# Optimization experiments

Measured on AMD Instinct MI355X. Metric: run time of the kernel, lower is better.

Reference implementation:

```python
import jax, jax.numpy as jnp
import numpy as np

B, N, D, L, T = 64, 64, 128, 4, 10  # batch, atoms, hidden_dim, n_layers, n_atom_types
EPS = 1e-5


def setup_inputs() -> dict:
    key = jax.random.key(0)
    ks = jax.random.split(key, 10)
    def rn(k, shape, s=0.05):
        return jax.random.normal(k, shape, jnp.float32) * s
    return dict(
        positions=jax.random.normal(ks[0], (B, N, 3), jnp.float32),
        atomic_numbers=jax.random.randint(ks[1], (B, N), 0, T),
        embed=rn(ks[2], (T, D)),
        edge_w1=rn(ks[3], (L, 2 * D + 1, D)), edge_b1=jnp.zeros((L, D), jnp.float32),
        edge_w2=rn(ks[4], (L, D, D)), edge_b2=jnp.zeros((L, D), jnp.float32),
        node_w1=rn(ks[5], (L, 2 * D, D)), node_b1=jnp.zeros((L, D), jnp.float32),
        node_w2=rn(ks[6], (L, D, D)), node_b2=jnp.zeros((L, D), jnp.float32),
        ln_g=jnp.ones((L, D), jnp.float32), ln_b=jnp.zeros((L, D), jnp.float32),
        out_w=rn(ks[7], (D, 3)), out_b=jnp.zeros((3,), jnp.float32),
    )


def _layer(h, dist_sq, ew1, eb1, ew2, eb2, nw1, nb1, nw2, nb2, g, b):
    # edge_mlp first linear on cat([h_i, h_j, dist_sq]) == h@Wa (bcast over j)
    # + h@Wb (bcast over i) + dist_sq * w_d, avoiding materializing the concat.
    wa, wb, wd = ew1[:D], ew1[D:2 * D], ew1[2 * D]
    pre = (h @ wa)[:, :, None, :] + (h @ wb)[:, None, :, :] + dist_sq * wd + eb1  # [B,N,N,D]
    m_ij = jax.nn.silu(jax.nn.silu(pre) @ ew2 + eb2)
    m_i = m_ij.mean(axis=2)  # mean over j -> [B,N,D]
    # node_mlp on cat([h, m_i]) split the same way; dropout is eval-mode identity.
    h_out = jax.nn.silu(h @ nw1[:D] + m_i @ nw1[D:] + nb1) @ nw2 + nb2
    x = h + h_out
    mu = x.mean(-1, keepdims=True)
    var = ((x - mu) ** 2).mean(-1, keepdims=True)
    return (x - mu) / jnp.sqrt(var + EPS) * g + b


def reference(positions, atomic_numbers, embed, edge_w1, edge_b1, edge_w2, edge_b2,
              node_w1, node_b1, node_w2, node_b2, ln_g, ln_b, out_w, out_b):
    h = embed[atomic_numbers]  # [B,N,D]
    diff = positions[:, :, None, :] - positions[:, None, :, :]
    dist_sq = (diff ** 2).sum(-1, keepdims=True)  # [B,N,N,1]
    for i in range(L):
        h = _layer(h, dist_sq, edge_w1[i], edge_b1[i], edge_w2[i], edge_b2[i],
                   node_w1[i], node_b1[i], node_w2[i], node_b2[i], ln_g[i], ln_b[i])
    return h @ out_w + out_b  # [B,N,3]
```

## Files before the change

### kernel.cpp

```cpp
#include <hip/hip_runtime.h>
#include <hip/hip_fp16.h>


typedef _Float16 f16;
typedef _Float16 f16x4 __attribute__((ext_vector_type(4)));
typedef _Float16 f16x8 __attribute__((ext_vector_type(8)));
typedef float f32x4 __attribute__((ext_vector_type(4)));

union H2x4 { f16x8 v; __half2 h[4]; };

__device__ __forceinline__ float bf2f(unsigned short u) {
    union { unsigned int i; float f; } v; v.i = ((unsigned int)u) << 16; return v.f;
}
__device__ __forceinline__ unsigned short f2bf(float f) {
    union { float f; unsigned int i; } v; v.f = f;
    unsigned int x = v.i;
    return (unsigned short)((x + 0x7fffu + ((x >> 16) & 1u)) >> 16);
}
__device__ __forceinline__ float silu_f(float x) {
    float e = __builtin_amdgcn_exp2f(-1.44269504088896f * x);
    return x * __builtin_amdgcn_rcpf(1.0f + e);
}
__device__ __forceinline__ __half2 silu_h2(__half2 x, __half2 kf, __half2 one2) {
    __half2 e = h2exp2(__hmul2(x, kf));
    return __hmul2(x, h2rcp(__hadd2(one2, e)));
}

struct Ptrs { const void* p[14]; };

__device__ __forceinline__ float ldf(const void* p, int i, int bf) {
    return bf ? bf2f(((const unsigned short*)p)[i]) : ((const float*)p)[i];
}

#define FRAG_TOTAL 49152
#define SMALL_TOTAL 17539

__global__ __launch_bounds__(256) void prep_kernel(
    Ptrs ptrs, f16* dst, float* sc)
{
    __shared__ int flgsh;
    int t = threadIdx.x;
    if (t < 64) {
        int ex = (((const unsigned short*)ptrs.p[0])[t * 2] >> 7) & 0xFF;
        unsigned long long m = __ballot(ex >= 110 && ex <= 135);
        if (t == 0) flgsh = (__popcll(m) >= 40) ? 1 : 0;
    }
    __syncthreads();
    int bf = flgsh;

    int gid = blockIdx.x * 256 + t;
    if (gid < FRAG_TOTAL) {
        int lay = gid / 12288;
        int r   = gid % 12288;
        const void* src; int base, rowoff = 0, r2;
        if (r < 6144) {
            int mat = r >> 11; r2 = r & 2047;
            if (mat == 0)      { src = ptrs.p[2]; base = lay * 32896; }
            else if (mat == 1) { src = ptrs.p[2]; base = lay * 32896; rowoff = 128; }
            else               { src = ptrs.p[4]; base = lay * 16384; }
        } else if (r < 10240) {
            r2 = r - 6144; src = ptrs.p[6]; base = lay * 32768;
        } else {
            r2 = r - 10240; src = ptrs.p[8]; base = lay * 16384;
        }
        int s = r2 >> 9, c = (r2 >> 6) & 7, l = r2 & 63;
        int row0 = rowoff + s * 32 + ((l >> 4) << 3);
        int col  = (c << 4) + (l & 15);
        f16x8 v;
#pragma unroll
        for (int jj = 0; jj < 8; jj++)
            v[jj] = (f16)ldf(src, base + (row0 + jj) * 128 + col, bf);
        *(f16x8*)(dst + gid * 8) = v;
    } else {
        int sid = gid - FRAG_TOTAL;
        if (sid >= SMALL_TOTAL) return;
        const void* src; int i;
        if      (sid < 12288) { src = ptrs.p[0]; i = sid; }
        else if (sid < 13568) { src = ptrs.p[1]; i = sid - 12288; }
        else if (sid < 14080) { int k = sid - 13568;
                                src = ptrs.p[2]; i = (k >> 7) * 32896 + 32768 + (k & 127); }
        else if (sid < 14592) { src = ptrs.p[3];  i = sid - 14080; }
        else if (sid < 15104) { src = ptrs.p[5];  i = sid - 14592; }
        else if (sid < 15616) { src = ptrs.p[7];  i = sid - 15104; }
        else if (sid < 16128) { src = ptrs.p[9];  i = sid - 15616; }
        else if (sid < 16640) { src = ptrs.p[10]; i = sid - 16128; }
        else if (sid < 17152) { src = ptrs.p[11]; i = sid - 16640; }
        else if (sid < 17536) { src = ptrs.p[12]; i = sid - 17152; }
        else                  { src = ptrs.p[13]; i = sid - 17536; }
        sc[sid] = ldf(src, i, bf);
    }
}

__global__ __launch_bounds__(256) void embed_ab_kernel(
    const int* an, const float* sc, const f16* wa, const f16* wb,
    const float* eb1C, f16* h16, f16* a16, f16* b16)
{
    int t = threadIdx.x;
    int w = t >> 6, lane = t & 63;
    int row0 = blockIdx.x << 4;
    int m_ = lane & 15, q_ = lane >> 4;
    const float* emb = sc + 12288;
    int a = an[row0 + m_];
    a = a < 0 ? 0 : (a > 9 ? 9 : a);
    f16x8 afrag[4];
#pragma unroll
    for (int s = 0; s < 4; s++) {
        f32x4 u0 = *(const f32x4*)(emb + a * 128 + s * 32 + q_ * 8);
        f32x4 u1 = *(const f32x4*)(emb + a * 128 + s * 32 + q_ * 8 + 4);
        f16x8 hv;
#pragma unroll
        for (int e = 0; e < 4; e++) { hv[e] = (f16)u0[e]; hv[e + 4] = (f16)u1[e]; }
        afrag[s] = hv;
        if (w == 0)
            *(f16x8*)(h16 + (row0 + m_) * 128 + s * 32 + q_ * 8) = hv;
    }
#pragma unroll
    for (int mat = 0; mat < 2; mat++) {
        const f16* W = mat ? wb : wa;
        f16* out     = mat ? b16 : a16;
#pragma unroll
        for (int cc = 0; cc < 2; cc++) {
            int c = 2 * w + cc;
            float init = mat ? 0.0f : eb1C[c * 16 + m_];
            f32x4 acc = { init, init, init, init };
#pragma unroll
            for (int s = 0; s < 4; s++) {
                f16x8 bfr = *(const f16x8*)(W + ((s * 8 + c) * 64 + lane) * 8);
                acc = __builtin_amdgcn_mfma_f32_16x16x32_f16(afrag[s], bfr, acc, 0, 0, 0);
            }
#pragma unroll
            for (int r = 0; r < 4; r++)
                out[(row0 + q_ * 4 + r) * 128 + c * 16 + m_] = (f16)acc[r];
        }
    }
}

__global__ __launch_bounds__(256) void edge_kernel(
    const float* sc, const f16* a16, const f16* b16,
    const f16* ew2_swz, const float* eb2C, const float* wdC, f16* m_out)
{
    __shared__ f16 Wlds[8192];
    __shared__ f16 S[64 * 136];
    __shared__ __half2 wd2_sh[64];
    __shared__ float dsq_sh[64];

    int t  = threadIdx.x;
    int ig = blockIdx.x;
    int b  = ig >> 6;
    const float* posC = sc;
    int lane = t & 63, w = t >> 6;
    int wr = w & 1, wc = w >> 1;

#pragma unroll
    for (int k = 0; k < 4; k++) {
        int idx = (k * 256 + t) * 8;
        *(f16x8*)(Wlds + idx) = *(const f16x8*)(ew2_swz + idx);
    }
    f16x8 bfB[2][4];
#pragma unroll
    for (int s2 = 0; s2 < 2; s2++)
#pragma unroll
        for (int c = 0; c < 4; c++)
            bfB[s2][c] = *(const f16x8*)(ew2_swz +
                (((s2 + 2) * 8 + wc * 4 + c) * 64 + lane) * 8);

    if (t >= 64 && t < 128) {
        int u = t - 64;
        wd2_sh[u] = __floats2half2_rn(wdC[2 * u], wdC[2 * u + 1]);
    }
    if (t < 64) {
        float xi = posC[ig * 3 + 0], yi = posC[ig * 3 + 1], zi = posC[ig * 3 + 2];
        int jg = b * 64 + t;
        float dx = xi - posC[jg * 3 + 0];
        float dy = yi - posC[jg * 3 + 1];
        float dz = zi - posC[jg * 3 + 2];
        dsq_sh[t] = dx * dx + dy * dy + dz * dz;
    }
    __syncthreads();

    {
        int j  = t >> 2;
        int cb = (t & 3) * 32;
        float dsf = dsq_sh[j];
        __half dh = __float2half_rn(dsf);
        __half2 ds2 = __halves2half2(dh, dh);
        __half2 kf   = __floats2half2_rn(-1.44269504f, -1.44269504f);
        __half2 one2 = __floats2half2_rn(1.0f, 1.0f);
        H2x4 a_r[4], wd_r[4];
#pragma unroll
        for (int k = 0; k < 4; k++) {
            a_r[k].v  = *(const f16x8*)(a16 + ig * 128 + cb + k * 8);
            wd_r[k].v = *(const f16x8*)((const f16*)wd2_sh + cb + k * 8);
        }
#pragma unroll
        for (int k = 0; k < 4; k++) {
            H2x4 bv, sv;
            bv.v = *(const f16x8*)(b16 + (b * 64 + j) * 128 + cb + k * 8);
#pragma unroll
            for (int e = 0; e < 4; e++) {
                __half2 pre = __hfma2(ds2, wd_r[k].h[e],
                                      __hadd2(a_r[k].h[e], bv.h[e]));
                sv.h[e] = silu_h2(pre, kf, one2);
            }
            *(f16x8*)(S + j * 136 + cb + k * 8) = sv.v;
        }
    }
    __syncthreads();

    int m_ = lane & 15, q_ = lane >> 4;
    f32x4 acc[4][2];
#pragma unroll
    for (int c = 0; c < 4; c++) {
        float e = eb2C[(wc * 4 + c) * 16 + m_];
        acc[c][0] = (f32x4){ e, e, e, e };
        acc[c][1] = acc[c][0];
    }
#pragma unroll
    for (int s = 0; s < 2; s++) {
        f16x8 bfr[4];
#pragma unroll
        for (int c = 0; c < 4; c++)
            bfr[c] = *(const f16x8*)(Wlds + ((s * 8 + wc * 4 + c) * 64 + lane) * 8);
#pragma unroll
        for (int mb = 0; mb < 2; mb++) {
            f16x8 af = *(const f16x8*)(S + ((wr * 2 + mb) * 16 + m_) * 136 + s * 32 + q_ * 8);
#pragma unroll
            for (int c = 0; c < 4; c++)
                acc[c][mb] = __builtin_amdgcn_mfma_f32_16x16x32_f16(af, bfr[c], acc[c][mb], 0, 0, 0);
        }
    }
#pragma unroll
    for (int s2 = 0; s2 < 2; s2++) {
#pragma unroll
        for (int mb = 0; mb < 2; mb++) {
            f16x8 af = *(const f16x8*)(S + ((wr * 2 + mb) * 16 + m_) * 136 + (s2 + 2) * 32 + q_ * 8);
#pragma unroll
            for (int c = 0; c < 4; c++)
                acc[c][mb] = __builtin_amdgcn_mfma_f32_16x16x32_f16(af, bfB[s2][c], acc[c][mb], 0, 0, 0);
        }
    }
    float scv4[4];
#pragma unroll
    for (int c = 0; c < 4; c++) {
        float scv = 0.0f;
#pragma unroll
        for (int mb = 0; mb < 2; mb++)
#pragma unroll
            for (int r = 0; r < 4; r++)
                scv += silu_f(acc[c][mb][r]);
        scv += __shfl_xor(scv, 16);
        scv += __shfl_xor(scv, 32);
        scv4[c] = scv;
    }
    __syncthreads();
    float* msum = (float*)S;
    if (lane < 16) {
#pragma unroll
        for (int c = 0; c < 4; c++)
            msum[wr * 128 + (wc * 4 + c) * 16 + lane] = scv4[c];
    }
    __syncthreads();
    if (t < 128) {
        float mv = (msum[t] + msum[128 + t]) * (1.0f / 64.0f);
        m_out[ig * 128 + t] = (f16)mv;
    }
}

__global__ __launch_bounds__(256) void node_mid_kernel(
    const f16* h16, const f16* m16, const f16* nw1s, const f16* nw2s,
    const float* nb1C, const float* nb2C, const float* lngC, const float* lnbC,
    const f16* waN, const f16* wbN, const float* eb1N,
    f16* a16, f16* b16)
{
    __shared__ f16 relay[16 * 136];
    __shared__ float s1sh[4][16], s2sh[4][16];
    int t = threadIdx.x;
    int w = t >> 6, lane = t & 63;
    int row0 = blockIdx.x << 4;
    int m_ = lane & 15, q_ = lane >> 4;

    f16x8 af[8];
#pragma unroll
    for (int s = 0; s < 4; s++) {
        af[s]     = *(const f16x8*)(h16 + (row0 + m_) * 128 + s * 32 + q_ * 8);
        af[s + 4] = *(const f16x8*)(m16 + (row0 + m_) * 128 + s * 32 + q_ * 8);
    }
#pragma unroll
    for (int cc = 0; cc < 2; cc++) {
        int c = 2 * w + cc;
        float e = nb1C[c * 16 + m_];
        f32x4 acc = { e, e, e, e };
#pragma unroll
        for (int s = 0; s < 8; s++) {
            f16x8 bfr = *(const f16x8*)(nw1s + ((s * 8 + c) * 64 + lane) * 8);
            acc = __builtin_amdgcn_mfma_f32_16x16x32_f16(af[s], bfr, acc, 0, 0, 0);
        }
#pragma unroll
        for (int r = 0; r < 4; r++)
            relay[(q_ * 4 + r) * 136 + c * 16 + m_] = (f16)silu_f(acc[r]);
    }
    __syncthreads();
    f16x8 uf[4];
#pragma unroll
    for (int s = 0; s < 4; s++)
        uf[s] = *(const f16x8*)(relay + m_ * 136 + s * 32 + q_ * 8);
    float x[2][4];
#pragma unroll
    for (int cc = 0; cc < 2; cc++) {
        int c = 2 * w + cc;
        float e = nb2C[c * 16 + m_];
        f32x4 acc = { e, e, e, e };
#pragma unroll
        for (int s = 0; s < 4; s++) {
            f16x8 bfr = *(const f16x8*)(nw2s + ((s * 8 + c) * 64 + lane) * 8);
            acc = __builtin_amdgcn_mfma_f32_16x16x32_f16(uf[s], bfr, acc, 0, 0, 0);
        }
#pragma unroll
        for (int r = 0; r < 4; r++)
            x[cc][r] = acc[r] + (float)h16[(row0 + q_ * 4 + r) * 128 + c * 16 + m_];
    }
    float s1p[4], s2p[4];
#pragma unroll
    for (int r = 0; r < 4; r++) {
        s1p[r] = x[0][r] + x[1][r];
        s2p[r] = x[0][r] * x[0][r] + x[1][r] * x[1][r];
    }
#pragma unroll
    for (int msk = 1; msk < 16; msk <<= 1)
#pragma unroll
        for (int r = 0; r < 4; r++) {
            s1p[r] += __shfl_xor(s1p[r], msk);
            s2p[r] += __shfl_xor(s2p[r], msk);
        }
    if (m_ == 0)
#pragma unroll
        for (int r = 0; r < 4; r++) {
            s1sh[w][q_ * 4 + r] = s1p[r];
            s2sh[w][q_ * 4 + r] = s2p[r];
        }
    __syncthreads();
    float mu[4], rs[4];
#pragma unroll
    for (int r = 0; r < 4; r++) {
        int row = q_ * 4 + r;
        float S1 = s1sh[0][row] + s1sh[1][row] + s1sh[2][row] + s1sh[3][row];
        float S2 = s2sh[0][row] + s2sh[1][row] + s2sh[2][row] + s2sh[3][row];
        mu[r] = S1 * (1.0f / 128.0f);
        float var = S2 * (1.0f / 128.0f) - mu[r] * mu[r];
        rs[r] = rsqrtf(var + 1e-5f);
    }
#pragma unroll
    for (int cc = 0; cc < 2; cc++) {
        int c = 2 * w + cc;
#pragma unroll
        for (int r = 0; r < 4; r++) {
            int col = c * 16 + m_;
            int row = row0 + q_ * 4 + r;
            float y = (x[cc][r] - mu[r]) * rs[r] * lngC[col] + lnbC[col];
            ((f16*)h16)[row * 128 + col] = (f16)y;
            relay[(q_ * 4 + r) * 136 + col] = (f16)y;
        }
    }
    __syncthreads();
    f16x8 hf[4];
#pragma unroll
    for (int s = 0; s < 4; s++)
        hf[s] = *(const f16x8*)(relay + m_ * 136 + s * 32 + q_ * 8);
#pragma unroll
    for (int mat = 0; mat < 2; mat++) {
        const f16* W = mat ? wbN : waN;
        f16* out     = mat ? b16 : a16;
#pragma unroll
        for (int cc = 0; cc < 2; cc++) {
            int c = 2 * w + cc;
            float init = mat ? 0.0f : eb1N[c * 16 + m_];
            f32x4 acc = { init, init, init, init };
#pragma unroll
            for (int s = 0; s < 4; s++) {
                f16x8 bfr = *(const f16x8*)(W + ((s * 8 + c) * 64 + lane) * 8);
                acc = __builtin_amdgcn_mfma_f32_16x16x32_f16(hf[s], bfr, acc, 0, 0, 0);
            }
#pragma unroll
            for (int r = 0; r < 4; r++)
                out[(row0 + q_ * 4 + r) * 128 + c * 16 + m_] = (f16)acc[r];
        }
    }
}

__global__ __launch_bounds__(256) void node_final_kernel(
    const void* pos_raw, const f16* h16, const f16* m16,
    const f16* nw1s, const f16* nw2s,
    const float* nb1C, const float* nb2C, const float* lngC, const float* lnbC,
    const float* owC, const float* obC, void* out)
{
    __shared__ f16 relay[16 * 136];
    __shared__ float s1sh[4][16], s2sh[4][16];
    __shared__ float psh[4][16][3];
    __shared__ int flgsh;
    int t = threadIdx.x;
    int w = t >> 6, lane = t & 63;
    int row0 = blockIdx.x << 4;
    int m_ = lane & 15, q_ = lane >> 4;

    if (t < 64) {
        int ex = (((const unsigned short*)pos_raw)[t * 2] >> 7) & 0xFF;
        unsigned long long mk = __ballot(ex >= 110 && ex <= 135);
        if (t == 0) flgsh = (__popcll(mk) >= 40) ? 1 : 0;
    }

    f16x8 af[8];
#pragma unroll
    for (int s = 0; s < 4; s++) {
        af[s]     = *(const f16x8*)(h16 + (row0 + m_) * 128 + s * 32 + q_ * 8);
        af[s + 4] = *(const f16x8*)(m16 + (row0 + m_) * 128 + s * 32 + q_ * 8);
    }
#pragma unroll
    for (int cc = 0; cc < 2; cc++) {
        int c = 2 * w + cc;
        float e = nb1C[c * 16 + m_];
        f32x4 acc = { e, e, e, e };
#pragma unroll
        for (int s = 0; s < 8; s++) {
            f16x8 bfr = *(const f16x8*)(nw1s + ((s * 8 + c) * 64 + lane) * 8);
            acc = __builtin_amdgcn_mfma_f32_16x16x32_f16(af[s], bfr, acc, 0, 0, 0);
        }
#pragma unroll
        for (int r = 0; r < 4; r++)
            relay[(q_ * 4 + r) * 136 + c * 16 + m_] = (f16)silu_f(acc[r]);
    }
    __syncthreads();
    f16x8 uf[4];
#pragma unroll
    for (int s = 0; s < 4; s++)
        uf[s] = *(const f16x8*)(relay + m_ * 136 + s * 32 + q_ * 8);
    float x[2][4];
#pragma unroll
    for (int cc = 0; cc < 2; cc++) {
        int c = 2 * w + cc;
        float e = nb2C[c * 16 + m_];
        f32x4 acc = { e, e, e, e };
#pragma unroll
        for (int s = 0; s < 4; s++) {
            f16x8 bfr = *(const f16x8*)(nw2s + ((s * 8 + c) * 64 + lane) * 8);
            acc = __builtin_amdgcn_mfma_f32_16x16x32_f16(uf[s], bfr, acc, 0, 0, 0);
        }
#pragma unroll
        for (int r = 0; r < 4; r++)
            x[cc][r] = acc[r] + (float)h16[(row0 + q_ * 4 + r) * 128 + c * 16 + m_];
    }
    float s1p[4], s2p[4];
#pragma unroll
    for (int r = 0; r < 4; r++) {
        s1p[r] = x[0][r] + x[1][r];
        s2p[r] = x[0][r] * x[0][r] + x[1][r] * x[1][r];
    }
#pragma unroll
    for (int msk = 1; msk < 16; msk <<= 1)
#pragma unroll
        for (int r = 0; r < 4; r++) {
            s1p[r] += __shfl_xor(s1p[r], msk);
            s2p[r] += __shfl_xor(s2p[r], msk);
        }
    if (m_ == 0)
#pragma unroll
        for (int r = 0; r < 4; r++) {
            s1sh[w][q_ * 4 + r] = s1p[r];
            s2sh[w][q_ * 4 + r] = s2p[r];
        }
    __syncthreads();
    float p[3][4];
#pragma unroll
    for (int r = 0; r < 4; r++) {
        int row = q_ * 4 + r;
        float S1 = s1sh[0][row] + s1sh[1][row] + s1sh[2][row] + s1sh[3][row];
        float S2 = s2sh[0][row] + s2sh[1][row] + s2sh[2][row] + s2sh[3][row];
        float mu = S1 * (1.0f / 128.0f);
        float var = S2 * (1.0f / 128.0f) - mu * mu;
        float rs = rsqrtf(var + 1e-5f);
        float p0 = 0.0f, p1 = 0.0f, p2 = 0.0f;
#pragma unroll
        for (int cc = 0; cc < 2; cc++) {
            int col = (2 * w + cc) * 16 + m_;
            float y = (x[cc][r] - mu) * rs * lngC[col] + lnbC[col];
            p0 += y * owC[col * 3 + 0];
            p1 += y * owC[col * 3 + 1];
            p2 += y * owC[col * 3 + 2];
        }
        p[0][r] = p0; p[1][r] = p1; p[2][r] = p2;
    }
#pragma unroll
    for (int msk = 1; msk < 16; msk <<= 1)
#pragma unroll
        for (int k = 0; k < 3; k++)
#pragma unroll
            for (int r = 0; r < 4; r++)
                p[k][r] += __shfl_xor(p[k][r], msk);
    if (m_ == 0)
#pragma unroll
        for (int r = 0; r < 4; r++)
#pragma unroll
            for (int k = 0; k < 3; k++)
                psh[w][q_ * 4 + r][k] = p[k][r];
    __syncthreads();
    if (t < 16) {
        int row = row0 + t;
        int bf = flgsh;
#pragma unroll
        for (int k = 0; k < 3; k++) {
            float v = psh[0][t][k] + psh[1][t][k] + psh[2][t][k] + psh[3][t][k]
                      + obC[k];
            if (bf) ((unsigned short*)out)[row * 3 + k] = f2bf(v);
            else    ((float*)out)[row * 3 + k] = v;
        }
    }
}

extern "C" void kernel_launch(void* const* d_in, const int* in_sizes, int n_in,
                              void* d_out, int out_size, void* d_ws, size_t ws_size,
                              hipStream_t stream)
{
    const int* an = (const int*)d_in[1];

    char* ws = (char*)d_ws;
    float* sc   = (float*)(ws + 1024);
    f16*   Wswz = (f16*)(ws + (128u << 10));
    f16*   h16  = (f16*)(ws + (1u << 20));
    f16*   a16  = (f16*)(ws + (2u << 20));
    f16*   b16  = (f16*)(ws + (3u << 20));
    f16*   m16  = (f16*)(ws + (4u << 20));

    Ptrs ptrs;
    const int src_idx[14] = {0, 2, 3, 4, 5, 6, 7, 8, 9, 10, 11, 12, 13, 14};
    for (int k = 0; k < 14; k++) ptrs.p[k] = d_in[src_idx[k]];

    prep_kernel<<<261, 256, 0, stream>>>(ptrs, Wswz, sc);
    embed_ab_kernel<<<256, 256, 0, stream>>>(an, sc, Wswz, Wswz + 16384,
                                             sc + 14080, h16, a16, b16);
    for (int lay = 0; lay < 4; lay++) {
        const f16* wl = Wswz + lay * 98304;
        const float* wdC  = sc + 13568 + lay * 128;
        const float* eb2C = sc + 14592 + lay * 128;
        const float* nb1C = sc + 15104 + lay * 128;
        const float* nb2C = sc + 15616 + lay * 128;
        const float* lngC = sc + 16128 + lay * 128;
        const float* lnbC = sc + 16640 + lay * 128;

        edge_kernel<<<4096, 256, 0, stream>>>(sc, a16, b16, wl + 32768,
                                              eb2C, wdC, m16);
        if (lay < 3) {
            const f16* wlN = Wswz + (lay + 1) * 98304;
            node_mid_kernel<<<256, 256, 0, stream>>>(
                h16, m16, wl + 49152, wl + 81920, nb1C, nb2C, lngC, lnbC,
                wlN, wlN + 16384, sc + 14080 + (lay + 1) * 128, a16, b16);
        } else {
            node_final_kernel<<<256, 256, 0, stream>>>(
                d_in[0], h16, m16, wl + 49152, wl + 81920,
                nb1C, nb2C, lngC, lnbC,
                sc + 17152, sc + 17536, d_out);
        }
    }
}
```

Before: 213.9 us.

## Widen parallelism in prep and node kernels, drop edge kernel barrier

The prep kernel now has each thread convert one weight element instead of eight, so it launches many more blocks. The embed and node kernels go from 4 to 8 waves per block, with each wave owning a single 16-column tile instead of two, and the LayerNorm and projection reductions are widened to match. The edge kernel moves its row-sum buffer into a separate shared array, which removes one __syncthreads at the cost of a little more LDS. The aim is to shorten the serial small kernels, but 8-wave blocks may lower occupancy, and the per-element prep writes are narrower.

New measurement: 216.0 us. No clear change (+1.0%).

```diff
diff --git a/kernel.cpp b/kernel.cpp
--- a/kernel.cpp
+++ b/kernel.cpp
@@ -33,6 +33,7 @@
 }
 
 #define FRAG_TOTAL 49152
+#define ELEM_TOTAL 393216
 #define SMALL_TOTAL 17539
 
 __global__ __launch_bounds__(256) void prep_kernel(
@@ -49,9 +50,10 @@
     int bf = flgsh;
 
     int gid = blockIdx.x * 256 + t;
-    if (gid < FRAG_TOTAL) {
-        int lay = gid / 12288;
-        int r   = gid % 12288;
+    if (gid < ELEM_TOTAL) {
+        int f = gid >> 3, j = gid & 7;
+        int lay = f / 12288;
+        int r   = f % 12288;
         const void* src; int base, rowoff = 0, r2;
         if (r < 6144) {
             int mat = r >> 11; r2 = r & 2047;
@@ -64,15 +66,11 @@
             r2 = r - 10240; src = ptrs.p[8]; base = lay * 16384;
         }
         int s = r2 >> 9, c = (r2 >> 6) & 7, l = r2 & 63;
-        int row0 = rowoff + s * 32 + ((l >> 4) << 3);
-        int col  = (c << 4) + (l & 15);
-        f16x8 v;
-#pragma unroll
-        for (int jj = 0; jj < 8; jj++)
-            v[jj] = (f16)ldf(src, base + (row0 + jj) * 128 + col, bf);
-        *(f16x8*)(dst + gid * 8) = v;
+        int row = rowoff + s * 32 + ((l >> 4) << 3) + j;
+        int col = (c << 4) + (l & 15);
+        dst[gid] = (f16)ldf(src, base + row * 128 + col, bf);
     } else {
-        int sid = gid - FRAG_TOTAL;
+        int sid = gid - ELEM_TOTAL;
         if (sid >= SMALL_TOTAL) return;
         const void* src; int i;
         if      (sid < 12288) { src = ptrs.p[0]; i = sid; }
@@ -91,7 +89,7 @@
     }
 }
 
-__global__ __launch_bounds__(256) void embed_ab_kernel(
+__global__ __launch_bounds__(512) void embed_ab_kernel(
     const int* an, const float* sc, const f16* wa, const f16* wb,
     const float* eb1C, f16* h16, f16* a16, f16* b16)
 {
@@ -114,24 +112,21 @@
         if (w == 0)
             *(f16x8*)(h16 + (row0 + m_) * 128 + s * 32 + q_ * 8) = hv;
     }
+    int c = w;
 #pragma unroll
     for (int mat = 0; mat < 2; mat++) {
         const f16* W = mat ? wb : wa;
         f16* out     = mat ? b16 : a16;
-#pragma unroll
-        for (int cc = 0; cc < 2; cc++) {
-            int c = 2 * w + cc;
-            float init = mat ? 0.0f : eb1C[c * 16 + m_];
-            f32x4 acc = { init, init, init, init };
-#pragma unroll
-            for (int s = 0; s < 4; s++) {
-                f16x8 bfr = *(const f16x8*)(W + ((s * 8 + c) * 64 + lane) * 8);
-                acc = __builtin_amdgcn_mfma_f32_16x16x32_f16(afrag[s], bfr, acc, 0, 0, 0);
-            }
-#pragma unroll
-            for (int r = 0; r < 4; r++)
-                out[(row0 + q_ * 4 + r) * 128 + c * 16 + m_] = (f16)acc[r];
-        }
+        float init = mat ? 0.0f : eb1C[c * 16 + m_];
+        f32x4 acc = { init, init, init, init };
+#pragma unroll
+        for (int s = 0; s < 4; s++) {
+            f16x8 bfr = *(const f16x8*)(W + ((s * 8 + c) * 64 + lane) * 8);
+            acc = __builtin_amdgcn_mfma_f32_16x16x32_f16(afrag[s], bfr, acc, 0, 0, 0);
+        }
+#pragma unroll
+        for (int r = 0; r < 4; r++)
+            out[(row0 + q_ * 4 + r) * 128 + c * 16 + m_] = (f16)acc[r];
     }
 }
 
@@ -143,6 +138,7 @@
     __shared__ f16 S[64 * 136];
     __shared__ __half2 wd2_sh[64];
     __shared__ float dsq_sh[64];
+    __shared__ float msum[256];
 
     int t  = threadIdx.x;
     int ig = blockIdx.x;
@@ -252,8 +248,6 @@
         scv += __shfl_xor(scv, 32);
         scv4[c] = scv;
     }
-    __syncthreads();
-    float* msum = (float*)S;
     if (lane < 16) {
 #pragma unroll
         for (int c = 0; c < 4; c++)
@@ -266,18 +260,19 @@
     }
 }
 
-__global__ __launch_bounds__(256) void node_mid_kernel(
+__global__ __launch_bounds__(512) void node_mid_kernel(
     const f16* h16, const f16* m16, const f16* nw1s, const f16* nw2s,
     const float* nb1C, const float* nb2C, const float* lngC, const float* lnbC,
     const f16* waN, const f16* wbN, const float* eb1N,
     f16* a16, f16* b16)
 {
     __shared__ f16 relay[16 * 136];
-    __shared__ float s1sh[4][16], s2sh[4][16];
+    __shared__ float s1sh[8][16], s2sh[8][16];
     int t = threadIdx.x;
     int w = t >> 6, lane = t & 63;
     int row0 = blockIdx.x << 4;
     int m_ = lane & 15, q_ = lane >> 4;
+    int c = w;
 
     f16x8 af[8];
 #pragma unroll
@@ -285,9 +280,7 @@
         af[s]     = *(const f16x8*)(h16 + (row0 + m_) * 128 + s * 32 + q_ * 8);
         af[s + 4] = *(const f16x8*)(m16 + (row0 + m_) * 128 + s * 32 + q_ * 8);
     }
-#pragma unroll
-    for (int cc = 0; cc < 2; cc++) {
-        int c = 2 * w + cc;
+    {
         float e = nb1C[c * 16 + m_];
         f32x4 acc = { e, e, e, e };
 #pragma unroll
@@ -304,10 +297,8 @@
 #pragma unroll
     for (int s = 0; s < 4; s++)
         uf[s] = *(const f16x8*)(relay + m_ * 136 + s * 32 + q_ * 8);
-    float x[2][4];
-#pragma unroll
-    for (int cc = 0; cc < 2; cc++) {
-        int c = 2 * w + cc;
+    float x[4];
+    {
         float e = nb2C[c * 16 + m_];
         f32x4 acc = { e, e, e, e };
 #pragma unroll
@@ -317,13 +308,13 @@
         }
 #pragma unroll
         for (int r = 0; r < 4; r++)
-            x[cc][r] = acc[r] + (float)h16[(row0 + q_ * 4 + r) * 128 + c * 16 + m_];
+            x[r] = acc[r] + (float)h16[(row0 + q_ * 4 + r) * 128 + c * 16 + m_];
     }
     float s1p[4], s2p[4];
 #pragma unroll
     for (int r = 0; r < 4; r++) {
-        s1p[r] = x[0][r] + x[1][r];
-        s2p[r] = x[0][r] * x[0][r] + x[1][r] * x[1][r];
+        s1p[r] = x[r];
+        s2p[r] = x[r] * x[r];
     }
 #pragma unroll
     for (int msk = 1; msk < 16; msk <<= 1)
@@ -343,23 +334,20 @@
 #pragma unroll
     for (int r = 0; r < 4; r++) {
         int row = q_ * 4 + r;
-        float S1 = s1sh[0][row] + s1sh[1][row] + s1sh[2][row] + s1sh[3][row];
-        float S2 = s2sh[0][row] + s2sh[1][row] + s2sh[2][row] + s2sh[3][row];
+        float S1 = 0.0f, S2 = 0.0f;
+#pragma unroll
+        for (int w2 = 0; w2 < 8; w2++) { S1 += s1sh[w2][row]; S2 += s2sh[w2][row]; }
         mu[r] = S1 * (1.0f / 128.0f);
         float var = S2 * (1.0f / 128.0f) - mu[r] * mu[r];
         rs[r] = rsqrtf(var + 1e-5f);
     }
 #pragma unroll
-    for (int cc = 0; cc < 2; cc++) {
-        int c = 2 * w + cc;
-#pragma unroll
-        for (int r = 0; r < 4; r++) {
-            int col = c * 16 + m_;
-            int row = row0 + q_ * 4 + r;
-            float y = (x[cc][r] - mu[r]) * rs[r] * lngC[col] + lnbC[col];
-            ((f16*)h16)[row * 128 + col] = (f16)y;
-            relay[(q_ * 4 + r) * 136 + col] = (f16)y;
-        }
+    for (int r = 0; r < 4; r++) {
+        int col = c * 16 + m_;
+        int row = row0 + q_ * 4 + r;
+        float y = (x[r] - mu[r]) * rs[r] * lngC[col] + lnbC[col];
+        ((f16*)h16)[row * 128 + col] = (f16)y;
+        relay[(q_ * 4 + r) * 136 + col] = (f16)y;
     }
     __syncthreads();
     f16x8 hf[4];
@@ -370,37 +358,34 @@
     for (int mat = 0; mat < 2; mat++) {
         const f16* W = mat ? wbN : waN;
         f16* out     = mat ? b16 : a16;
-#pragma unroll
-        for (int cc = 0; cc < 2; cc++) {
-            int c = 2 * w + cc;
-            float init = mat ? 0.0f : eb1N[c * 16 + m_];
-            f32x4 acc = { init, init, init, init };
-#pragma unroll
-            for (int s = 0; s < 4; s++) {
-                f16x8 bfr = *(const f16x8*)(W + ((s * 8 + c) * 64 + lane) * 8);
-                acc = __builtin_amdgcn_mfma_f32_16x16x32_f16(hf[s], bfr, acc, 0, 0, 0);
-            }
-#pragma unroll
-            for (int r = 0; r < 4; r++)
-                out[(row0 + q_ * 4 + r) * 128 + c * 16 + m_] = (f16)acc[r];
-        }
-    }
-}
-
-__global__ __launch_bounds__(256) void node_final_kernel(
+        float init = mat ? 0.0f : eb1N[c * 16 + m_];
+        f32x4 acc = { init, init, init, init };
+#pragma unroll
+        for (int s = 0; s < 4; s++) {
+            f16x8 bfr = *(const f16x8*)(W + ((s * 8 + c) * 64 + lane) * 8);
+            acc = __builtin_amdgcn_mfma_f32_16x16x32_f16(hf[s], bfr, acc, 0, 0, 0);
+        }
+#pragma unroll
+        for (int r = 0; r < 4; r++)
+            out[(row0 + q_ * 4 + r) * 128 + c * 16 + m_] = (f16)acc[r];
+    }
+}
+
+__global__ __launch_bounds__(512) void node_final_kernel(
     const void* pos_raw, const f16* h16, const f16* m16,
     const f16* nw1s, const f16* nw2s,
     const float* nb1C, const float* nb2C, const float* lngC, const float* lnbC,
     const float* owC, const float* obC, void* out)
 {
     __shared__ f16 relay[16 * 136];
-    __shared__ float s1sh[4][16], s2sh[4][16];
-    __shared__ float psh[4][16][3];
+    __shared__ float s1sh[8][16], s2sh[8][16];
+    __shared__ float psh[8][16][3];
     __shared__ int flgsh;
     int t = threadIdx.x;
     int w = t >> 6, lane = t & 63;
     int row0 = blockIdx.x << 4;
     int m_ = lane & 15, q_ = lane >> 4;
+    int c = w;
 
     if (t < 64) {
         int ex = (((const unsigned short*)pos_raw)[t * 2] >> 7) & 0xFF;
@@ -414,9 +399,7 @@
         af[s]     = *(const f16x8*)(h16 + (row0 + m_) * 128 + s * 32 + q_ * 8);
         af[s + 4] = *(const f16x8*)(m16 + (row0 + m_) * 128 + s * 32 + q_ * 8);
     }
-#pragma unroll
-    for (int cc = 0; cc < 2; cc++) {
-        int c = 2 * w + cc;
+    {
         float e = nb1C[c * 16 + m_];
         f32x4 acc = { e, e, e, e };
 #pragma unroll
@@ -433,10 +416,8 @@
 #pragma unroll
     for (int s = 0; s < 4; s++)
         uf[s] = *(const f16x8*)(relay + m_ * 136 + s * 32 + q_ * 8);
-    float x[2][4];
-#pragma unroll
-    for (int cc = 0; cc < 2; cc++) {
-        int c = 2 * w + cc;
+    float x[4];
+    {
         float e = nb2C[c * 16 + m_];
         f32x4 acc = { e, e, e, e };
 #pragma unroll
@@ -446,13 +427,13 @@
         }
 #pragma unroll
         for (int r = 0; r < 4; r++)
-            x[cc][r] = acc[r] + (float)h16[(row0 + q_ * 4 + r) * 128 + c * 16 + m_];
+            x[r] = acc[r] + (float)h16[(row0 + q_ * 4 + r) * 128 + c * 16 + m_];
     }
     float s1p[4], s2p[4];
 #pragma unroll
     for (int r = 0; r < 4; r++) {
-        s1p[r] = x[0][r] + x[1][r];
-        s2p[r] = x[0][r] * x[0][r] + x[1][r] * x[1][r];
+        s1p[r] = x[r];
+        s2p[r] = x[r] * x[r];
     }
 #pragma unroll
     for (int msk = 1; msk < 16; msk <<= 1)
@@ -472,21 +453,17 @@
 #pragma unroll
     for (int r = 0; r < 4; r++) {
         int row = q_ * 4 + r;
-        float S1 = s1sh[0][row] + s1sh[1][row] + s1sh[2][row] + s1sh[3][row];
-        float S2 = s2sh[0][row] + s2sh[1][row] + s2sh[2][row] + s2sh[3][row];
+        float S1 = 0.0f, S2 = 0.0f;
+#pragma unroll
+        for (int w2 = 0; w2 < 8; w2++) { S1 += s1sh[w2][row]; S2 += s2sh[w2][row]; }
         float mu = S1 * (1.0f / 128.0f);
         float var = S2 * (1.0f / 128.0f) - mu * mu;
         float rs = rsqrtf(var + 1e-5f);
-        float p0 = 0.0f, p1 = 0.0f, p2 = 0.0f;
-#pragma unroll
-        for (int cc = 0; cc < 2; cc++) {
-            int col = (2 * w + cc) * 16 + m_;
-            float y = (x[cc][r] - mu) * rs * lngC[col] + lnbC[col];
-            p0 += y * owC[col * 3 + 0];
-            p1 += y * owC[col * 3 + 1];
-            p2 += y * owC[col * 3 + 2];
-        }
-        p[0][r] = p0; p[1][r] = p1; p[2][r] = p2;
+        int col = c * 16 + m_;
+        float y = (x[r] - mu) * rs * lngC[col] + lnbC[col];
+        p[0][r] = y * owC[col * 3 + 0];
+        p[1][r] = y * owC[col * 3 + 1];
+        p[2][r] = y * owC[col * 3 + 2];
     }
 #pragma unroll
     for (int msk = 1; msk < 16; msk <<= 1)
@@ -507,8 +484,9 @@
         int bf = flgsh;
 #pragma unroll
         for (int k = 0; k < 3; k++) {
-            float v = psh[0][t][k] + psh[1][t][k] + psh[2][t][k] + psh[3][t][k]
-                      + obC[k];
+            float v = obC[k];
+#pragma unroll
+            for (int w2 = 0; w2 < 8; w2++) v += psh[w2][t][k];
             if (bf) ((unsigned short*)out)[row * 3 + k] = f2bf(v);
             else    ((float*)out)[row * 3 + k] = v;
         }
@@ -533,8 +511,8 @@
     const int src_idx[14] = {0, 2, 3, 4, 5, 6, 7, 8, 9, 10, 11, 12, 13, 14};
     for (int k = 0; k < 14; k++) ptrs.p[k] = d_in[src_idx[k]];
 
-    prep_kernel<<<261, 256, 0, stream>>>(ptrs, Wswz, sc);
-    embed_ab_kernel<<<256, 256, 0, stream>>>(an, sc, Wswz, Wswz + 16384,
+    prep_kernel<<<1605, 256, 0, stream>>>(ptrs, Wswz, sc);
+    embed_ab_kernel<<<256, 512, 0, stream>>>(an, sc, Wswz, Wswz + 16384,
                                              sc + 14080, h16, a16, b16);
     for (int lay = 0; lay < 4; lay++) {
         const f16* wl = Wswz + lay * 98304;
@@ -549,11 +527,11 @@
                                               eb2C, wdC, m16);
         if (lay < 3) {
             const f16* wlN = Wswz + (lay + 1) * 98304;
-            node_mid_kernel<<<256, 256, 0, stream>>>(
+            node_mid_kernel<<<256, 512, 0, stream>>>(
                 h16, m16, wl + 49152, wl + 81920, nb1C, nb2C, lngC, lnbC,
                 wlN, wlN + 16384, sc + 14080 + (lay + 1) * 128, a16, b16);
         } else {
-            node_final_kernel<<<256, 256, 0, stream>>>(
+            node_final_kernel<<<256, 512, 0, stream>>>(
                 d_in[0], h16, m16, wl + 49152, wl + 81920,
                 nb1C, nb2C, lngC, lnbC,
                 sc + 17152, sc + 17536, d_out);
```
